# Kernel optimization log

Measured on AMD Instinct MI355X. Metric: run time of the kernel, lower is better.

## Reference

```python
import jax, jax.numpy as jnp
import numpy as np

B, C4, H, W = 2, 128, 128, 128
POOL_SIZE = 10


def setup_inputs() -> dict:
    key = jax.random.key(0)
    k1, k2, k3 = jax.random.split(key, 3)
    feature = jax.random.normal(k1, (B, C4, H, W), dtype=jnp.float32)
    K = H * W
    # valid boxes: x1<x2, y1<y2, inside the feature map
    xy1 = jax.random.uniform(k2, (B, K, 2), dtype=jnp.float32) * jnp.array([W * 0.5, H * 0.5], jnp.float32)
    wh = jax.random.uniform(k3, (B, K, 2), dtype=jnp.float32) * jnp.array([W * 0.45, H * 0.45], jnp.float32) + 1.0
    boxes = jnp.concatenate([xy1, xy1 + wh], axis=-1)  # [B, K, 4] = (x1,y1,x2,y2)
    return {"feature": feature, "boxes": boxes, "pool_size": POOL_SIZE}


def reference(feature, boxes, pool_size):
    # feature: [B, 4*C, H, W]; boxes: [B, K, 4]; output: [B, C, K, 4]
    Bn, C4n, Hn, Wn = feature.shape
    C = C4n // 4
    K = boxes.shape[1]
    P = pool_size + 1
    x1, y1, x2, y2 = (boxes[..., i] for i in range(4))  # each [B, K]
    t = jnp.arange(P, dtype=feature.dtype) / pool_size  # [P]
    sx = x1[..., None] + t * (x2 - x1)[..., None]  # [B, K, P] along-x samples
    sy = y1[..., None] + t * (y2 - y1)[..., None]  # [B, K, P] along-y samples
    cx1 = jnp.broadcast_to(x1[..., None], sx.shape)
    cx2 = jnp.broadcast_to(x2[..., None], sx.shape)
    cy1 = jnp.broadcast_to(y1[..., None], sy.shape)
    cy2 = jnp.broadcast_to(y2[..., None], sy.shape)
    # border order: 0=top (y=y1), 1=left (x=x1), 2=bottom (y=y2), 3=right (x=x2)
    xs = jnp.stack([sx, cx1, sx, cx2], axis=1)  # [B, 4, K, P]
    ys = jnp.stack([cy1, sy, cy2, sy], axis=1)  # [B, 4, K, P]

    valid = (xs > -1.0) & (xs < Wn) & (ys > -1.0) & (ys < Hn)
    x = jnp.clip(xs, 0.0, Wn - 1)
    y = jnp.clip(ys, 0.0, Hn - 1)
    x0 = jnp.floor(x).astype(jnp.int32)
    y0 = jnp.floor(y).astype(jnp.int32)
    x1i = jnp.minimum(x0 + 1, Wn - 1)
    y1i = jnp.minimum(y0 + 1, Hn - 1)
    lx = (x - x0)[:, :, None]  # [B, 4, 1, K, P]
    ly = (y - y0)[:, :, None]

    featf = feature.reshape(Bn, 4, C, Hn * Wn)  # channel group g feeds border g

    def gather(yi, xi):
        idx = (yi * Wn + xi).reshape(Bn, 4, 1, K * P)
        return jnp.take_along_axis(featf, idx, axis=3).reshape(Bn, 4, C, K, P)

    val = (gather(y0, x0) * (1 - ly) * (1 - lx)
           + gather(y0, x1i) * (1 - ly) * lx
           + gather(y1i, x0) * ly * (1 - lx)
           + gather(y1i, x1i) * ly * lx)
    val = jnp.where(valid[:, :, None], val, 0.0)
    out = val.max(axis=-1)  # max-pool over the P samples per border -> [B, 4, C, K]
    return out.transpose(0, 2, 3, 1)  # [B, C, K, 4]
```

## Files before the change

kernel.cpp:

```cpp
#include <hip/hip_runtime.h>
#include <math.h>

#define BN   2
#define CG   32
#define HH   128
#define WW   128
#define HWSZ (HH*WW)
#define KK   16384
#define TK   16

typedef float vf4 __attribute__((ext_vector_type(4)));
typedef _Float16 h8 __attribute__((ext_vector_type(8)));

__device__ inline unsigned int pack_h2(float a, float b) {
  unsigned short ua = __builtin_bit_cast(unsigned short, (_Float16)a);
  unsigned short ub = __builtin_bit_cast(unsigned short, (_Float16)b);
  return (unsigned int)ua | ((unsigned int)ub << 16);
}

__global__ __launch_bounds__(256) void transpose_f16_kernel(
    const float* __restrict__ feat, unsigned short* __restrict__ ws) {
  __shared__ uint2 lds[128 * 9];
  const int s  = blockIdx.y;
  const int i0 = blockIdx.x * 128;
  const int t  = threadIdx.x;

  const int iL = (t & 31) * 4;
  const int cq = t >> 5;

  const float* src = feat + (size_t)s * (CG * HWSZ) + i0 + iL;
  vf4 r[4];
#pragma unroll
  for (int cc = 0; cc < 4; ++cc)
    r[cc] = *(const vf4*)(src + (size_t)(cq * 4 + cc) * HWSZ);

#pragma unroll
  for (int ii = 0; ii < 4; ++ii) {
    uint2 q;
    q.x = pack_h2(r[0][ii], r[1][ii]);
    q.y = pack_h2(r[2][ii], r[3][ii]);
    lds[(iL + ii) * 9 + cq] = q;
  }
  __syncthreads();

  uint2* dst = (uint2*)(ws + ((size_t)s * HWSZ + i0) * CG);
  const int q2 = t & 7;
  const int ih = t >> 3;
#pragma unroll
  for (int it = 0; it < 4; ++it) {
    const int i = ih + 32 * it;
    dst[i * 8 + q2] = lds[i * 9 + q2];
  }
}

__global__ __launch_bounds__(256) void border_align_kernel(
    const unsigned short* __restrict__ wsu, const float* __restrict__ boxes,
    const int* __restrict__ psp, float* __restrict__ out) {
  __shared__ float bxs[TK * 4];
  __shared__ float stf[64];
  __shared__ float lmax[TK * 4 * 33];

  const int blk = blockIdx.x;
  const int b   = (blk >> 2) & 1;
  const int k0  = (((blk >> 3) << 2) | (blk & 3)) * TK;
  const int t   = threadIdx.x;
  const int ps  = *psp;

  if (t < TK * 4) bxs[t] = boxes[((size_t)b * KK + k0) * 4 + t];
  if (t < 64 && t <= ps) stf[t] = (float)t / (float)ps;
  __syncthreads();

  const int g   = t >> 6;
  const int oct = t & 3;
  const int kk  = (t >> 2) & 15;
  const bool horiz = (g & 1) == 0;
  const int mshift = horiz ? 0 : 7;
  const int fshift = horiz ? 7 : 0;

  const _Float16* slab = (const _Float16*)wsu
      + (size_t)(b * 4 + g) * (HWSZ * CG) + oct * 8;

  const float x1 = bxs[kk * 4 + 0], y1 = bxs[kk * 4 + 1];
  const float x2 = bxs[kk * 4 + 2], y2 = bxs[kk * 4 + 3];
  float mov_s, mov_d, fix;
  if (horiz) { mov_s = x1; mov_d = x2 - x1; fix = (g == 0) ? y1 : y2; }
  else       { mov_s = y1; mov_d = y2 - y1; fix = (g == 1) ? x1 : x2; }
  const bool fok = (fix > -1.0f) && (fix < 128.0f);
  const float fc = fminf(fmaxf(fix, 0.0f), 127.0f);
  const int f0 = (int)fc;
  const float lf = fc - (float)f0;
  const int f1 = min(f0 + 1, 127);
  const int bf0 = f0 << fshift;
  const int bf1 = f1 << fshift;

  h8 acc = (h8)(_Float16)(-65504.0f);

  float lm_c; bool ok_c; int bm0_c, bm1_c;
  auto coords = [&](int p, int& bm0, int& bm1, float& lm, bool& ok) {
    const float mov = fmaf(stf[p], mov_d, mov_s);
    ok = fok && (mov > -1.0f) && (mov < 128.0f);
    const float mc = fminf(fmaxf(mov, 0.0f), 127.0f);
    const int m0 = (int)mc;
    lm = mc - (float)m0;
    const int m1 = min(m0 + 1, 127);
    bm0 = m0 << mshift;
    bm1 = m1 << mshift;
  };

  coords(0, bm0_c, bm1_c, lm_c, ok_c);
  h8 q00 = *(const h8*)(slab + ((size_t)(bf0 + bm0_c) << 5));
  h8 q01 = *(const h8*)(slab + ((size_t)(bf0 + bm1_c) << 5));
  h8 q10 = *(const h8*)(slab + ((size_t)(bf1 + bm0_c) << 5));
  h8 q11 = *(const h8*)(slab + ((size_t)(bf1 + bm1_c) << 5));

  for (int p = 0; p <= ps; ++p) {
    const float lm = lm_c;
    const bool ok = ok_c;
    h8 f00 = q00, f01 = q01, f10 = q10, f11 = q11;
    if (p < ps) {
      coords(p + 1, bm0_c, bm1_c, lm_c, ok_c);
      q00 = *(const h8*)(slab + ((size_t)(bf0 + bm0_c) << 5));
      q01 = *(const h8*)(slab + ((size_t)(bf0 + bm1_c) << 5));
      q10 = *(const h8*)(slab + ((size_t)(bf1 + bm0_c) << 5));
      q11 = *(const h8*)(slab + ((size_t)(bf1 + bm1_c) << 5));
    }
    const _Float16 w00 = (_Float16)((1.0f - lf) * (1.0f - lm));
    const _Float16 w01 = (_Float16)((1.0f - lf) * lm);
    const _Float16 w10 = (_Float16)(lf * (1.0f - lm));
    const _Float16 w11 = (_Float16)(lf * lm);
    h8 v = f00 * w00 + f01 * w01 + f10 * w10 + f11 * w11;
    v = ok ? v : (h8)(_Float16)0.0f;
    acc = __builtin_elementwise_max(acc, v);
  }

  const int kg = kk * 4 + g;
#pragma unroll
  for (int j = 0; j < 8; ++j)
    lmax[kg * 33 + oct * 8 + j] = (float)acc[j];
  __syncthreads();

  const int kgq = t & 15;
  const int cb  = t >> 4;
#pragma unroll
  for (int it = 0; it < 2; ++it) {
    const int c = cb + 16 * it;
    vf4 v;
#pragma unroll
    for (int j = 0; j < 4; ++j)
      v[j] = lmax[(kgq * 4 + j) * 33 + c];
    vf4* dst = (vf4*)(out + ((size_t)(b * CG + c) * KK + k0) * 4 + kgq * 4);
    __builtin_nontemporal_store(v, dst);
  }
}

__global__ __launch_bounds__(128) void border_align_fallback(
    const float* __restrict__ base, const float* __restrict__ boxes,
    const int* __restrict__ psp, float* __restrict__ out) {
  const int blk = blockIdx.x;
  const int b = blk >> 10;
  const int t = threadIdx.x;
  const int g = t >> 5, c = t & 31;
  const int k0 = (blk & 1023) * 16;
  const int ps = *psp;
  const float psf = (float)ps;
  const float* slab = base + (size_t)(b * 4 + g) * (CG * HWSZ) + (size_t)c * HWSZ;
  for (int kk = 0; kk < 16; ++kk) {
    const int kbox = k0 + kk;
    const float x1 = boxes[((size_t)b * KK + kbox) * 4 + 0];
    const float y1 = boxes[((size_t)b * KK + kbox) * 4 + 1];
    const float x2 = boxes[((size_t)b * KK + kbox) * 4 + 2];
    const float y2 = boxes[((size_t)b * KK + kbox) * 4 + 3];
    float m = -INFINITY;
    for (int p = 0; p <= ps; ++p) {
      const float tf = (float)p / psf;
      float x, y;
      if      (g == 0) { x = x1 + tf * (x2 - x1); y = y1; }
      else if (g == 1) { x = x1; y = y1 + tf * (y2 - y1); }
      else if (g == 2) { x = x1 + tf * (x2 - x1); y = y2; }
      else             { x = x2; y = y1 + tf * (y2 - y1); }
      const bool valid = (x > -1.0f) && (x < 128.0f) && (y > -1.0f) && (y < 128.0f);
      const float xc = fminf(fmaxf(x, 0.0f), 127.0f);
      const float yc = fminf(fmaxf(y, 0.0f), 127.0f);
      const int x0 = (int)xc, y0 = (int)yc;
      const float lx = xc - (float)x0, ly = yc - (float)y0;
      const int x1i = min(x0 + 1, 127), y1i = min(y0 + 1, 127);
      const float f00 = slab[y0 * WW + x0],  f01 = slab[y0 * WW + x1i];
      const float f10 = slab[y1i * WW + x0], f11 = slab[y1i * WW + x1i];
      float v = f00 * (1 - ly) * (1 - lx) + f01 * (1 - ly) * lx
              + f10 * ly * (1 - lx) + f11 * ly * lx;
      v = valid ? v : 0.0f;
      m = fmaxf(m, v);
    }
    out[(((size_t)(b * CG + c)) * KK + kbox) * 4 + g] = m;
  }
}

extern "C" void kernel_launch(void* const* d_in, const int* in_sizes, int n_in,
                              void* d_out, int out_size, void* d_ws, size_t ws_size,
                              hipStream_t stream) {
  const float* feature = (const float*)d_in[0];
  const float* boxes   = (const float*)d_in[1];
  const int*   psp     = (const int*)d_in[2];
  float*       out     = (float*)d_out;

  const size_t need = (size_t)BN * 4 * CG * HWSZ * sizeof(unsigned short);
  if (ws_size >= need) {
    unsigned short* ws = (unsigned short*)d_ws;
    hipLaunchKernelGGL(transpose_f16_kernel, dim3(HWSZ / 128, BN * 4),
                       dim3(256), 0, stream, feature, ws);
    hipLaunchKernelGGL(border_align_kernel, dim3(BN * (KK / TK)), dim3(256), 0,
                       stream, ws, boxes, psp, out);
  } else {
    hipLaunchKernelGGL(border_align_fallback, dim3(BN * (KK / 16)), dim3(128), 0,
                       stream, feature, boxes, psp, out);
  }
}
```

Measured before the change: 96.28 us.

## Assign one border-slab per block and interleave slabs across blocks

Each border-align block now handles a single (batch, border) slab for 64 boxes, where before it covered all four borders for 16 boxes. Block indices interleave the 8 slabs so concurrently running blocks spread across all of them, and the transpose kernel uses the same interleaving. The aim is better cache locality per block, since each block touches only one feature slab. In exchange, output stores become scalar strided writes with stride 4 floats instead of vectorized float4 writes, which may hurt write coalescing.

After: 113.4 us. 1.18x slower.

```diff
diff --git a/kernel.cpp b/kernel.cpp
--- a/kernel.cpp
+++ b/kernel.cpp
@@ -7,7 +7,7 @@
 #define WW   128
 #define HWSZ (HH*WW)
 #define KK   16384
-#define TK   16
+#define TB   64
 
 typedef float vf4 __attribute__((ext_vector_type(4)));
 typedef _Float16 h8 __attribute__((ext_vector_type(8)));
@@ -21,8 +21,9 @@
 __global__ __launch_bounds__(256) void transpose_f16_kernel(
     const float* __restrict__ feat, unsigned short* __restrict__ ws) {
   __shared__ uint2 lds[128 * 9];
-  const int s  = blockIdx.y;
-  const int i0 = blockIdx.x * 128;
+  const int blk = blockIdx.x;
+  const int s  = blk & 7;
+  const int i0 = (blk >> 3) * 128;
   const int t  = threadIdx.x;
 
   const int iL = (t & 31) * 4;
@@ -56,29 +57,30 @@
 __global__ __launch_bounds__(256) void border_align_kernel(
     const unsigned short* __restrict__ wsu, const float* __restrict__ boxes,
     const int* __restrict__ psp, float* __restrict__ out) {
-  __shared__ float bxs[TK * 4];
+  __shared__ float bxs[TB * 4];
   __shared__ float stf[64];
-  __shared__ float lmax[TK * 4 * 33];
+  __shared__ float lmax[TB * 33];
 
   const int blk = blockIdx.x;
-  const int b   = (blk >> 2) & 1;
-  const int k0  = (((blk >> 3) << 2) | (blk & 3)) * TK;
+  const int s   = blk & 7;
+  const int b   = s >> 2;
+  const int g   = s & 3;
+  const int k0  = (blk >> 3) * TB;
   const int t   = threadIdx.x;
   const int ps  = *psp;
 
-  if (t < TK * 4) bxs[t] = boxes[((size_t)b * KK + k0) * 4 + t];
+  bxs[t] = boxes[((size_t)b * KK + k0) * 4 + t];
   if (t < 64 && t <= ps) stf[t] = (float)t / (float)ps;
   __syncthreads();
 
-  const int g   = t >> 6;
+  const int kk  = t >> 2;
   const int oct = t & 3;
-  const int kk  = (t >> 2) & 15;
   const bool horiz = (g & 1) == 0;
   const int mshift = horiz ? 0 : 7;
   const int fshift = horiz ? 7 : 0;
 
   const _Float16* slab = (const _Float16*)wsu
-      + (size_t)(b * 4 + g) * (HWSZ * CG) + oct * 8;
+      + (size_t)s * (HWSZ * CG) + oct * 8;
 
   const float x1 = bxs[kk * 4 + 0], y1 = bxs[kk * 4 + 1];
   const float x2 = bxs[kk * 4 + 2], y2 = bxs[kk * 4 + 3];
@@ -133,23 +135,18 @@
     acc = __builtin_elementwise_max(acc, v);
   }
 
-  const int kg = kk * 4 + g;
 #pragma unroll
   for (int j = 0; j < 8; ++j)
-    lmax[kg * 33 + oct * 8 + j] = (float)acc[j];
+    lmax[kk * 33 + oct * 8 + j] = (float)acc[j];
   __syncthreads();
 
-  const int kgq = t & 15;
-  const int cb  = t >> 4;
-#pragma unroll
-  for (int it = 0; it < 2; ++it) {
-    const int c = cb + 16 * it;
-    vf4 v;
-#pragma unroll
-    for (int j = 0; j < 4; ++j)
-      v[j] = lmax[(kgq * 4 + j) * 33 + c];
-    vf4* dst = (vf4*)(out + ((size_t)(b * CG + c) * KK + k0) * 4 + kgq * 4);
-    __builtin_nontemporal_store(v, dst);
+  const int kL = t & 63;
+  const int cb = t >> 6;
+  float* obase = out + ((size_t)b * CG * KK + (size_t)(k0 + kL)) * 4 + g;
+#pragma unroll
+  for (int it = 0; it < 8; ++it) {
+    const int c = cb + 4 * it;
+    __builtin_nontemporal_store(lmax[kL * 33 + c], obase + (size_t)c * KK * 4);
   }
 }
 
@@ -206,10 +203,10 @@
   const size_t need = (size_t)BN * 4 * CG * HWSZ * sizeof(unsigned short);
   if (ws_size >= need) {
     unsigned short* ws = (unsigned short*)d_ws;
-    hipLaunchKernelGGL(transpose_f16_kernel, dim3(HWSZ / 128, BN * 4),
+    hipLaunchKernelGGL(transpose_f16_kernel, dim3(8 * (HWSZ / 128)),
                        dim3(256), 0, stream, feature, ws);
-    hipLaunchKernelGGL(border_align_kernel, dim3(BN * (KK / TK)), dim3(256), 0,
-                       stream, ws, boxes, psp, out);
+    hipLaunchKernelGGL(border_align_kernel, dim3(BN * 4 * (KK / TB)), dim3(256),
+                       0, stream, ws, boxes, psp, out);
   } else {
     hipLaunchKernelGGL(border_align_fallback, dim3(BN * (KK / 16)), dim3(128), 0,
                        stream, feature, boxes, psp, out);
```

## Deepen gather prefetch to three samples and simplify block-to-box mapping

Applied to the files above, without the earlier changes.

Replaces the one-stage software prefetch of the four bilinear-corner loads with a three-deep rotating register pipeline, so more gather loads stay in flight while earlier samples are blended and max-reduced. It also changes the block index mapping to interleave batches (b = blk&1) instead of the previous grouped mapping, which changes which workspace slabs concurrently running blocks touch. The sample table is clamped for out-of-range entries so the speculative early issues read defined values. Keeping three stages live raises register pressure, which could lower occupancy.

Result: no change. 95.87 us (-0.4%).

```diff
diff --git a/kernel.cpp b/kernel.cpp
--- a/kernel.cpp
+++ b/kernel.cpp
@@ -61,13 +61,13 @@
   __shared__ float lmax[TK * 4 * 33];
 
   const int blk = blockIdx.x;
-  const int b   = (blk >> 2) & 1;
-  const int k0  = (((blk >> 3) << 2) | (blk & 3)) * TK;
+  const int b   = blk & 1;
+  const int k0  = (blk >> 1) * TK;
   const int t   = threadIdx.x;
   const int ps  = *psp;
 
   if (t < TK * 4) bxs[t] = boxes[((size_t)b * KK + k0) * 4 + t];
-  if (t < 64 && t <= ps) stf[t] = (float)t / (float)ps;
+  if (t < 64) stf[t] = (float)(t <= ps ? t : ps) / (float)ps;
   __syncthreads();
 
   const int g   = t >> 6;
@@ -95,43 +95,65 @@
 
   h8 acc = (h8)(_Float16)(-65504.0f);
 
-  float lm_c; bool ok_c; int bm0_c, bm1_c;
-  auto coords = [&](int p, int& bm0, int& bm1, float& lm, bool& ok) {
-    const float mov = fmaf(stf[p], mov_d, mov_s);
-    ok = fok && (mov > -1.0f) && (mov < 128.0f);
-    const float mc = fminf(fmaxf(mov, 0.0f), 127.0f);
-    const int m0 = (int)mc;
-    lm = mc - (float)m0;
-    const int m1 = min(m0 + 1, 127);
-    bm0 = m0 << mshift;
-    bm1 = m1 << mshift;
-  };
-
-  coords(0, bm0_c, bm1_c, lm_c, ok_c);
-  h8 q00 = *(const h8*)(slab + ((size_t)(bf0 + bm0_c) << 5));
-  h8 q01 = *(const h8*)(slab + ((size_t)(bf0 + bm1_c) << 5));
-  h8 q10 = *(const h8*)(slab + ((size_t)(bf1 + bm0_c) << 5));
-  h8 q11 = *(const h8*)(slab + ((size_t)(bf1 + bm1_c) << 5));
-
-  for (int p = 0; p <= ps; ++p) {
-    const float lm = lm_c;
-    const bool ok = ok_c;
-    h8 f00 = q00, f01 = q01, f10 = q10, f11 = q11;
-    if (p < ps) {
-      coords(p + 1, bm0_c, bm1_c, lm_c, ok_c);
-      q00 = *(const h8*)(slab + ((size_t)(bf0 + bm0_c) << 5));
-      q01 = *(const h8*)(slab + ((size_t)(bf0 + bm1_c) << 5));
-      q10 = *(const h8*)(slab + ((size_t)(bf1 + bm0_c) << 5));
-      q11 = *(const h8*)(slab + ((size_t)(bf1 + bm1_c) << 5));
-    }
-    const _Float16 w00 = (_Float16)((1.0f - lf) * (1.0f - lm));
-    const _Float16 w01 = (_Float16)((1.0f - lf) * lm);
-    const _Float16 w10 = (_Float16)(lf * (1.0f - lm));
-    const _Float16 w11 = (_Float16)(lf * lm);
-    h8 v = f00 * w00 + f01 * w01 + f10 * w10 + f11 * w11;
-    v = ok ? v : (h8)(_Float16)0.0f;
-    acc = __builtin_elementwise_max(acc, v);
-  }
+#define ISSUE(P, Q0, Q1, Q2, Q3, LM, OK) do {                              \
+    const float mov_ = fmaf(stf[(P)], mov_d, mov_s);                       \
+    OK = fok && (mov_ > -1.0f) && (mov_ < 128.0f);                         \
+    const float mc_ = fminf(fmaxf(mov_, 0.0f), 127.0f);                    \
+    const int m0_ = (int)mc_;                                              \
+    LM = mc_ - (float)m0_;                                                 \
+    const int m1_ = min(m0_ + 1, 127);                                     \
+    const int bm0_ = m0_ << mshift, bm1_ = m1_ << mshift;                  \
+    Q0 = *(const h8*)(slab + ((size_t)(bf0 + bm0_) << 5));                 \
+    Q1 = *(const h8*)(slab + ((size_t)(bf0 + bm1_) << 5));                 \
+    Q2 = *(const h8*)(slab + ((size_t)(bf1 + bm0_) << 5));                 \
+    Q3 = *(const h8*)(slab + ((size_t)(bf1 + bm1_) << 5));                 \
+  } while (0)
+
+#define CONSUME(Q0, Q1, Q2, Q3, LM, OK) do {                               \
+    const float lm_ = LM;                                                  \
+    const _Float16 w00 = (_Float16)((1.0f - lf) * (1.0f - lm_));           \
+    const _Float16 w01 = (_Float16)((1.0f - lf) * lm_);                    \
+    const _Float16 w10 = (_Float16)(lf * (1.0f - lm_));                    \
+    const _Float16 w11 = (_Float16)(lf * lm_);                             \
+    h8 v_ = Q0 * w00 + Q1 * w01 + Q2 * w10 + Q3 * w11;                     \
+    v_ = (OK) ? v_ : (h8)(_Float16)0.0f;                                   \
+    acc = __builtin_elementwise_max(acc, v_);                              \
+  } while (0)
+
+  h8 qA0, qA1, qA2, qA3, qB0, qB1, qB2, qB3, qC0, qC1, qC2, qC3;
+  float lmA, lmB, lmC;
+  bool okA, okB, okC;
+
+  ISSUE(0, qA0, qA1, qA2, qA3, lmA, okA);
+  ISSUE(1, qB0, qB1, qB2, qB3, lmB, okB);
+  ISSUE(2, qC0, qC1, qC2, qC3, lmC, okC);
+
+  int p = 0;
+  for (; p + 2 <= ps; p += 3) {
+    {
+      h8 f0 = qA0, f1 = qA1, f2 = qA2, f3 = qA3;
+      const float lm = lmA; const bool ok = okA;
+      if (p + 3 <= ps) ISSUE(p + 3, qA0, qA1, qA2, qA3, lmA, okA);
+      CONSUME(f0, f1, f2, f3, lm, ok);
+    }
+    {
+      h8 f0 = qB0, f1 = qB1, f2 = qB2, f3 = qB3;
+      const float lm = lmB; const bool ok = okB;
+      if (p + 4 <= ps) ISSUE(p + 4, qB0, qB1, qB2, qB3, lmB, okB);
+      CONSUME(f0, f1, f2, f3, lm, ok);
+    }
+    {
+      h8 f0 = qC0, f1 = qC1, f2 = qC2, f3 = qC3;
+      const float lm = lmC; const bool ok = okC;
+      if (p + 5 <= ps) ISSUE(p + 5, qC0, qC1, qC2, qC3, lmC, okC);
+      CONSUME(f0, f1, f2, f3, lm, ok);
+    }
+  }
+  if (p <= ps)     CONSUME(qA0, qA1, qA2, qA3, lmA, okA);
+  if (p + 1 <= ps) CONSUME(qB0, qB1, qB2, qB3, lmB, okB);
+
+#undef ISSUE
+#undef CONSUME
 
   const int kg = kk * 4 + g;
 #pragma unroll
```

## Bin boxes by fixed border row and gather bilinear samples from LDS tiles

Applied to the files above, without the earlier changes.

Each box border is bucketed by the integer coordinate of its fixed axis, using atomic counters. One block per bucket half stages the two needed feature rows (all 32 channels, f16) into swizzled LDS, then does every box's bilinear samples and max-pool from LDS instead of scattered global/L2 gathers. Results go to an f16 intermediate, and a separate untranspose kernel writes the [B,C,K,4] output. This adds three kernel launches, atomics, an extra round trip through memory and uneven per-bucket work. Any bucket holding more than CAP entries silently drops those boxes.

Measured after the change: 151.4 us. 1.57x slower.

```diff
diff --git a/kernel.cpp b/kernel.cpp
--- a/kernel.cpp
+++ b/kernel.cpp
@@ -7,7 +7,13 @@
 #define WW   128
 #define HWSZ (HH*WW)
 #define KK   16384
-#define TK   16
+#define CAP  1024
+
+#define WS_F16_OFF  (0u)
+#define WS_CNT_OFF  (8u << 20)
+#define WS_BKT_OFF  ((8u << 20) + 4096u)
+#define WS_TMP_OFF  (16u << 20)
+#define WS_NEED     (24u << 20)
 
 typedef float vf4 __attribute__((ext_vector_type(4)));
 typedef _Float16 h8 __attribute__((ext_vector_type(8)));
@@ -53,102 +59,153 @@
   }
 }
 
-__global__ __launch_bounds__(256) void border_align_kernel(
+__global__ void zero_cnt_kernel(unsigned int* __restrict__ cnt) {
+  cnt[blockIdx.x * blockDim.x + threadIdx.x] = 0u;
+}
+
+__global__ __launch_bounds__(256) void bin_kernel(
+    const float* __restrict__ boxes, unsigned int* __restrict__ cnt,
+    unsigned short* __restrict__ bkt) {
+  const int idx = blockIdx.x * 256 + threadIdx.x;
+  const int b = idx >> 14;
+  const int k = idx & (KK - 1);
+  const vf4 bx = *(const vf4*)(boxes + (size_t)idx * 4);
+#pragma unroll
+  for (int g = 0; g < 4; ++g) {
+    const float fix = (g == 0) ? bx[1] : (g == 1) ? bx[0]
+                     : (g == 2) ? bx[3] : bx[2];
+    const float fc = fminf(fmaxf(fix, 0.0f), 127.0f);
+    const int f0 = (int)fc;
+    const int bin = ((b * 4 + g) << 7) + f0;
+    const unsigned int slot = atomicAdd(&cnt[bin], 1u);
+    if (slot < CAP) bkt[(size_t)bin * CAP + slot] = (unsigned short)k;
+  }
+}
+
+__global__ __launch_bounds__(256) void border_gather_binned(
     const unsigned short* __restrict__ wsu, const float* __restrict__ boxes,
-    const int* __restrict__ psp, float* __restrict__ out) {
-  __shared__ float bxs[TK * 4];
+    const unsigned int* __restrict__ cnt, const unsigned short* __restrict__ bkt,
+    const int* __restrict__ psp, unsigned short* __restrict__ tmp) {
+  __shared__ _Float16 tile[2 * 128 * 32];
   __shared__ float stf[64];
-  __shared__ float lmax[TK * 4 * 33];
-
+
+  const int blk  = blockIdx.x;
+  const int sbin = blk >> 1;
+  const int h    = blk & 1;
+  const int f0   = sbin & 127;
+  const int g    = (sbin >> 7) & 3;
+  const int b    = sbin >> 9;
+  const int n    = min((int)cnt[sbin], CAP);
+  const int half = (n + 1) >> 1;
+  const int i0   = h * half;
+  const int i1   = min(n, i0 + half);
+  if (i1 <= i0) return;
+
+  const int t  = threadIdx.x;
+  const int ps = *psp;
+  if (t < 64) stf[t] = (float)(t <= ps ? t : ps) / (float)ps;
+
+  const bool horiz = (g & 1) == 0;
+  const int f1 = min(f0 + 1, 127);
+  const _Float16* slab = (const _Float16*)wsu + (size_t)(b * 4 + g) * (HWSZ * CG);
+
+#pragma unroll
+  for (int it = 0; it < 4; ++it) {
+    const int chunk = it * 256 + t;
+    const int cc   = chunk >> 9;
+    const int rem  = chunk & 511;
+    const int p    = rem >> 2;
+    const int slot = rem & 3;
+    const int fcc  = cc ? f1 : f0;
+    const size_t srci = horiz ? ((size_t)(fcc * 128 + p) * 32)
+                              : ((size_t)(p * 128 + fcc) * 32);
+    const uint4 v = *(const uint4*)(slab + srci + slot * 8);
+    const int slotS = slot ^ ((p >> 1) & 3);
+    *(uint4*)((char*)tile + cc * 8192 + p * 64 + slotS * 16) = v;
+  }
+  __syncthreads();
+
+  const int w      = t >> 6;
+  const int oct    = t & 3;
+  const int slot16 = (t >> 2) & 15;
+
+  for (int base = i0 + w * 16; base < i1; base += 64) {
+    const int ii  = base + slot16;
+    const bool vb = ii < i1;
+    const int kid = vb ? (int)bkt[(size_t)sbin * CAP + ii] : 0;
+    const vf4 bx  = *(const vf4*)(boxes + ((size_t)b * KK + kid) * 4);
+
+    float mov_s, mov_d, fix;
+    if (horiz) { mov_s = bx[0]; mov_d = bx[2] - bx[0]; fix = (g == 0) ? bx[1] : bx[3]; }
+    else       { mov_s = bx[1]; mov_d = bx[3] - bx[1]; fix = (g == 1) ? bx[0] : bx[2]; }
+    const bool fok = (fix > -1.0f) && (fix < 128.0f);
+    const float fc = fminf(fmaxf(fix, 0.0f), 127.0f);
+    const float lf = fc - (float)f0;
+
+    h8 acc = (h8)(_Float16)(-65504.0f);
+
+    for (int p = 0; p <= ps; ++p) {
+      const float mov = fmaf(stf[p], mov_d, mov_s);
+      const bool ok = fok && (mov > -1.0f) && (mov < 128.0f);
+      const float mc = fminf(fmaxf(mov, 0.0f), 127.0f);
+      const int m0 = (int)mc;
+      const float lm = mc - (float)m0;
+      const int m1 = min(m0 + 1, 127);
+      const int a0 = (m0 << 6) + ((oct ^ ((m0 >> 1) & 3)) << 4);
+      const int a1 = (m1 << 6) + ((oct ^ ((m1 >> 1) & 3)) << 4);
+      const h8 f00 = *(const h8*)((const char*)tile + a0);
+      const h8 f01 = *(const h8*)((const char*)tile + a1);
+      const h8 f10 = *(const h8*)((const char*)tile + 8192 + a0);
+      const h8 f11 = *(const h8*)((const char*)tile + 8192 + a1);
+      const _Float16 w00 = (_Float16)((1.0f - lf) * (1.0f - lm));
+      const _Float16 w01 = (_Float16)((1.0f - lf) * lm);
+      const _Float16 w10 = (_Float16)(lf * (1.0f - lm));
+      const _Float16 w11 = (_Float16)(lf * lm);
+      h8 v = f00 * w00 + f01 * w01 + f10 * w10 + f11 * w11;
+      v = ok ? v : (h8)(_Float16)0.0f;
+      acc = __builtin_elementwise_max(acc, v);
+    }
+
+    if (vb) {
+      h8* dst = (h8*)(tmp + ((size_t)(b * 4 + g) * KK + kid) * 32 + oct * 8);
+      __builtin_nontemporal_store(acc, dst);
+    }
+  }
+}
+
+__global__ __launch_bounds__(256) void untranspose_kernel(
+    const unsigned short* __restrict__ tmp, float* __restrict__ out) {
+  __shared__ float lds[4 * 32 * 33];
   const int blk = blockIdx.x;
-  const int b   = (blk >> 2) & 1;
-  const int k0  = (((blk >> 3) << 2) | (blk & 3)) * TK;
+  const int b   = blk >> 9;
+  const int k0  = (blk & 511) * 32;
   const int t   = threadIdx.x;
-  const int ps  = *psp;
-
-  if (t < TK * 4) bxs[t] = boxes[((size_t)b * KK + k0) * 4 + t];
-  if (t < 64 && t <= ps) stf[t] = (float)t / (float)ps;
+
+#pragma unroll
+  for (int it = 0; it < 2; ++it) {
+    const int chunk = it * 256 + t;
+    const int g   = chunk >> 7;
+    const int rem = chunk & 127;
+    const int kk  = rem >> 2;
+    const int co8 = rem & 3;
+    const h8 v = *(const h8*)((const _Float16*)tmp
+                 + ((size_t)(b * 4 + g) * KK + k0 + kk) * 32 + co8 * 8);
+#pragma unroll
+    for (int j = 0; j < 8; ++j)
+      lds[g * (32 * 33) + kk * 33 + co8 * 8 + j] = (float)v[j];
+  }
   __syncthreads();
 
-  const int g   = t >> 6;
-  const int oct = t & 3;
-  const int kk  = (t >> 2) & 15;
-  const bool horiz = (g & 1) == 0;
-  const int mshift = horiz ? 0 : 7;
-  const int fshift = horiz ? 7 : 0;
-
-  const _Float16* slab = (const _Float16*)wsu
-      + (size_t)(b * 4 + g) * (HWSZ * CG) + oct * 8;
-
-  const float x1 = bxs[kk * 4 + 0], y1 = bxs[kk * 4 + 1];
-  const float x2 = bxs[kk * 4 + 2], y2 = bxs[kk * 4 + 3];
-  float mov_s, mov_d, fix;
-  if (horiz) { mov_s = x1; mov_d = x2 - x1; fix = (g == 0) ? y1 : y2; }
-  else       { mov_s = y1; mov_d = y2 - y1; fix = (g == 1) ? x1 : x2; }
-  const bool fok = (fix > -1.0f) && (fix < 128.0f);
-  const float fc = fminf(fmaxf(fix, 0.0f), 127.0f);
-  const int f0 = (int)fc;
-  const float lf = fc - (float)f0;
-  const int f1 = min(f0 + 1, 127);
-  const int bf0 = f0 << fshift;
-  const int bf1 = f1 << fshift;
-
-  h8 acc = (h8)(_Float16)(-65504.0f);
-
-  float lm_c; bool ok_c; int bm0_c, bm1_c;
-  auto coords = [&](int p, int& bm0, int& bm1, float& lm, bool& ok) {
-    const float mov = fmaf(stf[p], mov_d, mov_s);
-    ok = fok && (mov > -1.0f) && (mov < 128.0f);
-    const float mc = fminf(fmaxf(mov, 0.0f), 127.0f);
-    const int m0 = (int)mc;
-    lm = mc - (float)m0;
-    const int m1 = min(m0 + 1, 127);
-    bm0 = m0 << mshift;
-    bm1 = m1 << mshift;
-  };
-
-  coords(0, bm0_c, bm1_c, lm_c, ok_c);
-  h8 q00 = *(const h8*)(slab + ((size_t)(bf0 + bm0_c) << 5));
-  h8 q01 = *(const h8*)(slab + ((size_t)(bf0 + bm1_c) << 5));
-  h8 q10 = *(const h8*)(slab + ((size_t)(bf1 + bm0_c) << 5));
-  h8 q11 = *(const h8*)(slab + ((size_t)(bf1 + bm1_c) << 5));
-
-  for (int p = 0; p <= ps; ++p) {
-    const float lm = lm_c;
-    const bool ok = ok_c;
-    h8 f00 = q00, f01 = q01, f10 = q10, f11 = q11;
-    if (p < ps) {
-      coords(p + 1, bm0_c, bm1_c, lm_c, ok_c);
-      q00 = *(const h8*)(slab + ((size_t)(bf0 + bm0_c) << 5));
-      q01 = *(const h8*)(slab + ((size_t)(bf0 + bm1_c) << 5));
-      q10 = *(const h8*)(slab + ((size_t)(bf1 + bm0_c) << 5));
-      q11 = *(const h8*)(slab + ((size_t)(bf1 + bm1_c) << 5));
-    }
-    const _Float16 w00 = (_Float16)((1.0f - lf) * (1.0f - lm));
-    const _Float16 w01 = (_Float16)((1.0f - lf) * lm);
-    const _Float16 w10 = (_Float16)(lf * (1.0f - lm));
-    const _Float16 w11 = (_Float16)(lf * lm);
-    h8 v = f00 * w00 + f01 * w01 + f10 * w10 + f11 * w11;
-    v = ok ? v : (h8)(_Float16)0.0f;
-    acc = __builtin_elementwise_max(acc, v);
-  }
-
-  const int kg = kk * 4 + g;
-#pragma unroll
-  for (int j = 0; j < 8; ++j)
-    lmax[kg * 33 + oct * 8 + j] = (float)acc[j];
-  __syncthreads();
-
-  const int kgq = t & 15;
-  const int cb  = t >> 4;
-#pragma unroll
-  for (int it = 0; it < 2; ++it) {
-    const int c = cb + 16 * it;
+#pragma unroll
+  for (int it = 0; it < 4; ++it) {
+    const int chunk = it * 256 + t;
+    const int c  = chunk >> 5;
+    const int kk = chunk & 31;
     vf4 v;
 #pragma unroll
-    for (int j = 0; j < 4; ++j)
-      v[j] = lmax[(kgq * 4 + j) * 33 + c];
-    vf4* dst = (vf4*)(out + ((size_t)(b * CG + c) * KK + k0) * 4 + kgq * 4);
+    for (int g = 0; g < 4; ++g)
+      v[g] = lds[g * (32 * 33) + kk * 33 + c];
+    vf4* dst = (vf4*)(out + ((size_t)(b * CG + c) * KK + k0 + kk) * 4);
     __builtin_nontemporal_store(v, dst);
   }
 }
@@ -203,13 +260,22 @@
   const int*   psp     = (const int*)d_in[2];
   float*       out     = (float*)d_out;
 
-  const size_t need = (size_t)BN * 4 * CG * HWSZ * sizeof(unsigned short);
-  if (ws_size >= need) {
-    unsigned short* ws = (unsigned short*)d_ws;
+  if (ws_size >= WS_NEED) {
+    char* ws = (char*)d_ws;
+    unsigned short* wsf16 = (unsigned short*)(ws + WS_F16_OFF);
+    unsigned int*   cnt   = (unsigned int*)(ws + WS_CNT_OFF);
+    unsigned short* bkt   = (unsigned short*)(ws + WS_BKT_OFF);
+    unsigned short* tmp   = (unsigned short*)(ws + WS_TMP_OFF);
+
     hipLaunchKernelGGL(transpose_f16_kernel, dim3(HWSZ / 128, BN * 4),
-                       dim3(256), 0, stream, feature, ws);
-    hipLaunchKernelGGL(border_align_kernel, dim3(BN * (KK / TK)), dim3(256), 0,
-                       stream, ws, boxes, psp, out);
+                       dim3(256), 0, stream, feature, wsf16);
+    hipLaunchKernelGGL(zero_cnt_kernel, dim3(1), dim3(1024), 0, stream, cnt);
+    hipLaunchKernelGGL(bin_kernel, dim3(BN * KK / 256), dim3(256), 0, stream,
+                       boxes, cnt, bkt);
+    hipLaunchKernelGGL(border_gather_binned, dim3(2 * 1024), dim3(256), 0,
+                       stream, wsf16, boxes, cnt, bkt, psp, tmp);
+    hipLaunchKernelGGL(untranspose_kernel, dim3(BN * 512), dim3(256), 0, stream,
+                       tmp, out);
   } else {
     hipLaunchKernelGGL(border_align_fallback, dim3(BN * (KK / 16)), dim3(128), 0,
                        stream, feature, boxes, psp, out);
```
